# Kernel tuning notes

Hardware: AMD Instinct MI355X
Metric: run time of the kernel (lower is better)

The kernel has to match this reference:

```python
import jax, jax.numpy as jnp
import numpy as np

B, T, U, V, C, K = 64, 800, 64, 60, 512, 10

def setup_inputs() -> dict:
    key = jax.random.key(0)
    ks = jax.random.split(key, 8)
    x = jax.random.normal(ks[0], (B, T, 3), dtype=jnp.float32)
    char_ids = jax.random.randint(ks[1], (B, U), 0, V)
    onehots = jax.nn.one_hot(char_ids, V, dtype=jnp.float32)  # [B,U,V]
    text_lens = jax.random.randint(ks[2], (B, 1), 32, U + 1).astype(jnp.float32)
    w_old = jnp.zeros((B, V), jnp.float32)
    kappa_old = jnp.zeros((B, K), jnp.float32)
    prev_h = jnp.zeros((B, C), jnp.float32)
    prev_c = jnp.zeros((B, C), jnp.float32)
    s = 0.08
    W_ih = jax.random.normal(ks[3], (4 * C, 3 + V), jnp.float32) * s
    W_hh = jax.random.normal(ks[4], (4 * C, C), jnp.float32) * s
    b_ih = jnp.zeros((4 * C,), jnp.float32)
    b_hh = jnp.zeros((4 * C,), jnp.float32)
    win_W = jax.random.normal(ks[5], (3 * K, C), jnp.float32) * s
    win_b = jnp.zeros((3 * K,), jnp.float32)
    return dict(x=x, onehots=onehots, text_lens=text_lens, w_old=w_old,
                kappa_old=kappa_old, prev_h=prev_h, prev_c=prev_c,
                W_ih=W_ih, W_hh=W_hh, b_ih=b_ih, b_hh=b_hh,
                win_W=win_W, win_b=win_b)

def reference(x, onehots, text_lens, w_old, kappa_old, prev_h, prev_c,
              W_ih, W_hh, b_ih, b_hh, win_W, win_b):
    Upad = onehots.shape[1]
    idx = jnp.arange(Upad + 1, dtype=x.dtype)          # text-position indices
    scale = Upad / text_lens                           # [B,1] length normalization

    def step(carry, xt):
        h, c, w, kap = carry
        inp = jnp.concatenate([xt, w], axis=-1)        # [B, 3+V]
        gates = inp @ W_ih.T + b_ih + h @ W_hh.T + b_hh
        i, f, g, o = jnp.split(gates, 4, axis=-1)
        i = jax.nn.sigmoid(i); f = jax.nn.sigmoid(f)
        g = jnp.tanh(g);      o = jax.nn.sigmoid(o)
        c = f * c + i * g
        h = o * jnp.tanh(c)
        # Gaussian-mixture attention window
        p = jnp.exp(h @ win_W.T + win_b)               # [B, 3K]
        alpha, beta, dkap = jnp.split(p, 3, axis=-1)   # each [B, K]
        kap = kap + dkap
        gravity = -beta[:, :, None] * (kap[:, :, None] - idx) ** 2   # [B,K,U+1]
        phi = jnp.sum(alpha[:, :, None] * jnp.exp(gravity), axis=1) * scale  # [B,U+1]
        w = jnp.einsum('bu,buv->bv', phi[:, :Upad], onehots)
        return (h, c, w, kap), (h, w, phi)

    xs = jnp.swapaxes(x, 0, 1)                         # [T,B,3]
    (h, c, w, kap), (hs, ws, phis) = jax.lax.scan(
        step, (prev_h, prev_c, w_old, kappa_old), xs)
    ws = jnp.swapaxes(ws, 0, 1)                        # [B,T,V]
    hs = jnp.swapaxes(hs, 0, 1)                        # [B,T,C]
    return ws, hs, h, c, w, kap, phis[-1]
```

## Files before the change

kernel.cpp:

```cpp
#include <hip/hip_runtime.h>
#include <math.h>

#define B_  64
#define T_  800
#define U_  64
#define V_  60
#define C_  512
#define K_  10
#define KXF 584
#define NWG 256
#define NTH 512
#define KQ  8
#define KSL 72
#define NB  4
#define GRPWG 16

typedef unsigned long long ull;
typedef _Float16 f16;
typedef _Float16 f16x2 __attribute__((ext_vector_type(2)));

__device__ __forceinline__ float sigm(float v)  { return 1.f/(1.f+__expf(-v)); }
__device__ __forceinline__ float tanhx(float v) { return 1.f - 2.f/(__expf(2.f*v)+1.f); }

__device__ __forceinline__ ull ldp(const ull* p) {
  return __hip_atomic_load(p, __ATOMIC_RELAXED, __HIP_MEMORY_SCOPE_AGENT);
}
__device__ __forceinline__ float dot2(f16x2 a, f16x2 b, float c) {
  return __builtin_amdgcn_fdot2(a, b, c, false);
}
__device__ __forceinline__ f16x2 bc2(unsigned u) {
  return __builtin_bit_cast(f16x2, u);
}
__device__ __forceinline__ float wfetch(const float* __restrict__ W_ih,
                                        const float* __restrict__ W_hh,
                                        int row, int k) {
  if (k < 3)  return W_ih[row*63 + k];
  if (k == 3) return 0.f;
  if (k < 64) return W_ih[row*63 + (k-1)];
  return W_hh[row*C_ + (k-64)];
}

__global__ __launch_bounds__(NTH, 2)
void lstm_attn_persistent(
    const float* __restrict__ x,
    const float* __restrict__ onehots,
    const float* __restrict__ text_lens,
    const float* __restrict__ w_old,
    const float* __restrict__ kappa_old,
    const float* __restrict__ prev_h,
    const float* __restrict__ prev_c,
    const float* __restrict__ W_ih,
    const float* __restrict__ W_hh,
    const float* __restrict__ b_ih,
    const float* __restrict__ b_hh,
    const float* __restrict__ win_W,
    const float* __restrict__ win_b,
    ull* __restrict__ hpair,
    float* __restrict__ out)
{
  const long OUT_WS  = 0;
  const long OUT_HS  = (long)B_*T_*V_;
  const long OUT_H   = OUT_HS + (long)B_*T_*C_;
  const long OUT_C   = OUT_H  + (long)B_*C_;
  const long OUT_W   = OUT_C  + (long)B_*C_;
  const long OUT_KAP = OUT_W  + (long)B_*V_;
  const long OUT_PHI = OUT_KAP+ (long)B_*K_;

  const int tid  = threadIdx.x;
  const int kq   = tid >> 6;
  const int lane = tid & 63;
  const int bid  = blockIdx.x;
  const int grp  = bid & 15;
  const int gblk = bid >> 4;
  const int b0   = grp * NB;

  const int rlo = kq ? (kq*KSL - 64) : 0;
  const int rhi = kq*64 + 64;

  __shared__ __align__(16) f16   hxh[NB][KXF];
  __shared__ __align__(16) float wbuf[NB][64];
  __shared__ __align__(16) float part[KQ][NB][2][68];
  __shared__ __align__(16) float wpart[KQ][NB][68];
  __shared__ float p_lds[NB][32];
  __shared__ float kap_lds[NB][12];
  __shared__ float scale_lds[NB];
  __shared__ float winb_lds[32];
  __shared__ int   ids_lds[NB][64];

  f16x2 Wh[2][KSL/2];
  float bias2[2];
  #pragma unroll
  for (int s = 0; s < 2; ++s) {
    int gp   = gblk*128 + lane + 64*s;
    int gate = gp & 3;
    int ch   = gp >> 2;
    int row  = gate*C_ + ch;
    #pragma unroll
    for (int i = 0; i < KSL/2; ++i) {
      float w0 = wfetch(W_ih, W_hh, row, kq*KSL + 2*i);
      float w1 = wfetch(W_ih, W_hh, row, kq*KSL + 2*i + 1);
      f16x2 p; p[0] = (f16)w0; p[1] = (f16)w1;
      Wh[s][i] = p;
    }
    bias2[s] = b_ih[row] + b_hh[row];
  }

  const int wj = lane % 30;
  const int wh = (lane < 60) ? (lane / 30) : 0;
  f16x2 winh[16];
  #pragma unroll
  for (int i = 0; i < 16; ++i) {
    f16x2 p;
    p[0] = (f16)win_W[wj*C_ + kq*64 + wh*32 + 2*i];
    p[1] = (f16)win_W[wj*C_ + kq*64 + wh*32 + 2*i + 1];
    winh[i] = p;
  }

  const int ub    = tid >> 5;
  const int chloc = tid & 31;
  const int mych  = gblk*32 + chloc;
  float c_reg = 0.f;
  if (tid < 128) c_reg = prev_c[(long)(b0 + ub)*C_ + mych];

  for (int i = tid; i < NB*576; i += NTH) {
    int bb = i / 576, k = i % 576;
    int b = b0 + bb;
    float v;
    if      (k < 3)  v = x[((long)b*T_ + 0)*3 + k];
    else if (k < 4)  v = 0.f;
    else if (k < 64) v = w_old[b*V_ + (k-4)];
    else             v = prev_h[(long)b*C_ + (k-64)];
    hxh[bb][k] = (f16)v;
  }
  for (int i = tid; i < NB*64; i += NTH) {
    int bb = i >> 6, j = i & 63;
    wbuf[bb][j] = (j < 60) ? w_old[(b0+bb)*V_ + j] : 0.f;
  }
  for (int i = tid; i < NB*K_; i += NTH)
    kap_lds[i/K_][i%K_] = kappa_old[(b0 + i/K_)*K_ + i%K_];
  if (tid < NB) scale_lds[tid] = (float)U_ / text_lens[b0 + tid];
  if (tid < 30) winb_lds[tid] = win_b[tid];
  for (int i = tid; i < NB*U_; i += NTH) {
    int bb = i / U_, u = i % U_;
    const float* oh = onehots + ((long)(b0+bb)*U_ + u)*V_;
    int best = 0; float bv = oh[0];
    for (int vv = 1; vv < V_; ++vv) { float q = oh[vv]; if (q > bv) { bv = q; best = vv; } }
    ids_lds[bb][u] = best;
  }
  __syncthreads();

  for (int t = 0; t < T_; ++t) {
    float acc[NB][2];
    #pragma unroll
    for (int bb = 0; bb < NB; ++bb) {
      acc[bb][0] = (kq == 0) ? bias2[0] : 0.f;
      acc[bb][1] = (kq == 0) ? bias2[1] : 0.f;
    }
    #pragma unroll
    for (int bb = 0; bb < NB; ++bb) {
      const uint4* hb = (const uint4*)&hxh[bb][kq*KSL];
      float a0 = acc[bb][0], a1 = acc[bb][1];
      #pragma unroll
      for (int j = 0; j < 9; ++j) {
        uint4 hv = hb[j];
        f16x2 h0 = bc2(hv.x), h1 = bc2(hv.y), h2 = bc2(hv.z), h3 = bc2(hv.w);
        a0 = dot2(Wh[0][4*j+0], h0, a0);  a1 = dot2(Wh[1][4*j+0], h0, a1);
        a0 = dot2(Wh[0][4*j+1], h1, a0);  a1 = dot2(Wh[1][4*j+1], h1, a1);
        a0 = dot2(Wh[0][4*j+2], h2, a0);  a1 = dot2(Wh[1][4*j+2], h2, a1);
        a0 = dot2(Wh[0][4*j+3], h3, a0);  a1 = dot2(Wh[1][4*j+3], h3, a1);
      }
      acc[bb][0] = a0; acc[bb][1] = a1;
    }
    #pragma unroll
    for (int bb = 0; bb < NB; ++bb) {
      part[kq][bb][0][lane] = acc[bb][0];
      part[kq][bb][1][lane] = acc[bb][1];
    }
    __syncthreads();

    if (tid < 128) {
      const int sr = chloc >> 4, c4 = (chloc & 15) * 4;
      float4 s = make_float4(0.f, 0.f, 0.f, 0.f);
      #pragma unroll
      for (int q = 0; q < KQ; ++q) {
        float4 v = *(const float4*)&part[q][ub][sr][c4];
        s.x += v.x; s.y += v.y; s.z += v.z; s.w += v.w;
      }
      float ig = sigm(s.x), fg = sigm(s.y), gg = tanhx(s.z), og = sigm(s.w);
      float c = fg*c_reg + ig*gg;
      c_reg = c;
      float h = og * tanhx(c);
      int b = b0 + ub;
      ull pk = ((ull)(unsigned)(t+1) << 32) | (ull)__float_as_uint(h);
      __hip_atomic_store(&hpair[(long)(t&1)*B_*C_ + (long)b*C_ + mych], pk,
                         __ATOMIC_RELAXED, __HIP_MEMORY_SCOPE_AGENT);
      out[OUT_HS + ((long)b*T_ + t)*C_ + mych] = h;
      if (t == T_-1) {
        out[OUT_H + (long)b*C_ + mych] = h;
        out[OUT_C + (long)b*C_ + mych] = c;
      }
    }

    {
      const ull* src = hpair + (long)(t&1)*B_*C_;
      const int want = t + 1;
      const int ch = rlo + lane*2;
      const bool act = ch < rhi;
      const ull* q0 = src + (long)(b0+0)*C_ + ch;
      const ull* q1 = src + (long)(b0+1)*C_ + ch;
      const ull* q2 = src + (long)(b0+2)*C_ + ch;
      const ull* q3 = src + (long)(b0+3)*C_ + ch;
      ull a0=0,a1=0,c0=0,c1=0,e0=0,e1=0,g0=0,g1=0;
      while (true) {
        bool ok = true;
        if (act) {
          a0 = ldp(q0); a1 = ldp(q0+1);
          c0 = ldp(q1); c1 = ldp(q1+1);
          e0 = ldp(q2); e1 = ldp(q2+1);
          g0 = ldp(q3); g1 = ldp(q3+1);
          ok = (int)(a0>>32) >= want && (int)(a1>>32) >= want &&
               (int)(c0>>32) >= want && (int)(c1>>32) >= want &&
               (int)(e0>>32) >= want && (int)(e1>>32) >= want &&
               (int)(g0>>32) >= want && (int)(g1>>32) >= want;
        }
        if (__all(ok)) break;
      }
      if (act) {
        f16x2 p;
        p[0] = (f16)__uint_as_float((unsigned)a0);
        p[1] = (f16)__uint_as_float((unsigned)a1);
        *(unsigned*)&hxh[0][64+ch] = __builtin_bit_cast(unsigned, p);
        p[0] = (f16)__uint_as_float((unsigned)c0);
        p[1] = (f16)__uint_as_float((unsigned)c1);
        *(unsigned*)&hxh[1][64+ch] = __builtin_bit_cast(unsigned, p);
        p[0] = (f16)__uint_as_float((unsigned)e0);
        p[1] = (f16)__uint_as_float((unsigned)e1);
        *(unsigned*)&hxh[2][64+ch] = __builtin_bit_cast(unsigned, p);
        p[0] = (f16)__uint_as_float((unsigned)g0);
        p[1] = (f16)__uint_as_float((unsigned)g1);
        *(unsigned*)&hxh[3][64+ch] = __builtin_bit_cast(unsigned, p);
      }
    }

    #pragma unroll
    for (int bb = 0; bb < NB; ++bb) {
      const uint4* hb = (const uint4*)&hxh[bb][64 + kq*64 + wh*32];
      float a = 0.f;
      #pragma unroll
      for (int j = 0; j < 4; ++j) {
        uint4 hv = hb[j];
        a = dot2(winh[4*j+0], bc2(hv.x), a);
        a = dot2(winh[4*j+1], bc2(hv.y), a);
        a = dot2(winh[4*j+2], bc2(hv.z), a);
        a = dot2(winh[4*j+3], bc2(hv.w), a);
      }
      if (lane < 60) wpart[kq][bb][lane] = a;
    }
    __syncthreads();

    if (kq < NB) {
      const int bb = kq;
      if (lane < 30) {
        float s = 0.f;
        #pragma unroll
        for (int q = 0; q < KQ; ++q) s += wpart[q][bb][lane] + wpart[q][bb][30+lane];
        float p = __expf(s + winb_lds[lane]);
        p_lds[bb][lane] = p;
        if (lane >= 20) {
          float nk = kap_lds[bb][lane-20] + p;
          kap_lds[bb][lane-20] = nk;
          if (t == T_-1 && gblk == 0) out[OUT_KAP + (b0+bb)*K_ + (lane-20)] = nk;
        }
      }
      if (lane < 60) wbuf[bb][lane] = 0.f;
      else if (lane < 63) {
        int tn = t + 1;
        hxh[bb][lane-60] = (f16)((tn < T_) ? x[((long)(b0+bb)*T_ + tn)*3 + (lane-60)] : 0.f);
      }
      {
        float s = 0.f;
        float uf = (float)lane;
        #pragma unroll
        for (int k = 0; k < K_; ++k) {
          float d = kap_lds[bb][k] - uf;
          s += p_lds[bb][k] * __expf(-p_lds[bb][10+k]*d*d);
        }
        float phiv = s * scale_lds[bb];
        atomicAdd(&wbuf[bb][ids_lds[bb][lane]], phiv);
        if (t == T_-1 && gblk == 0) {
          out[OUT_PHI + (b0+bb)*65 + lane] = phiv;
          if (lane == 0) {
            float s2 = 0.f;
            #pragma unroll
            for (int k = 0; k < K_; ++k) {
              float d = kap_lds[bb][k] - 64.f;
              s2 += p_lds[bb][k] * __expf(-p_lds[bb][10+k]*d*d);
            }
            out[OUT_PHI + (b0+bb)*65 + 64] = s2 * scale_lds[bb];
          }
        }
      }
      if (lane < 60) {
        float wv = wbuf[bb][lane];
        hxh[bb][4+lane] = (f16)wv;
        if (gblk == (t & 15)) {
          out[OUT_WS + ((long)(b0+bb)*T_ + t)*V_ + lane] = wv;
          if (t == T_-1) out[OUT_W + (b0+bb)*V_ + lane] = wv;
        }
      }
    }
    __syncthreads();
  }
}

extern "C" void kernel_launch(void* const* d_in, const int* in_sizes, int n_in,
                              void* d_out, int out_size, void* d_ws, size_t ws_size,
                              hipStream_t stream) {
  const float* x         = (const float*)d_in[0];
  const float* onehots   = (const float*)d_in[1];
  const float* text_lens = (const float*)d_in[2];
  const float* w_old     = (const float*)d_in[3];
  const float* kappa_old = (const float*)d_in[4];
  const float* prev_h    = (const float*)d_in[5];
  const float* prev_c    = (const float*)d_in[6];
  const float* W_ih      = (const float*)d_in[7];
  const float* W_hh      = (const float*)d_in[8];
  const float* b_ih      = (const float*)d_in[9];
  const float* b_hh      = (const float*)d_in[10];
  const float* win_W     = (const float*)d_in[11];
  const float* win_b     = (const float*)d_in[12];
  ull*   hpair = (ull*)d_ws;
  float* out   = (float*)d_out;

  hipMemsetAsync(d_ws, 0, 2ull*B_*C_*sizeof(ull), stream);

  lstm_attn_persistent<<<NWG, NTH, 0, stream>>>(
      x, onehots, text_lens, w_old, kappa_old, prev_h, prev_c,
      W_ih, W_hh, b_ih, b_hh, win_W, win_b, hpair, out);
}
```

Before: 4.326 ms.

## Poll hidden-state exchange via XCD-local L2 with MALL fallback copy

Each h value is now written twice, once as a plain store to a local copy and once as an agent-scope atomic to a global copy. Consumers poll with inline-asm dwordx4 loads that carry sc0 (local L2 scope) and switch permanently to sc0 sc1 loads of the global copy after 200 failed tries. The goal is cheaper polling when producer and consumer share an XCD, plus vectorized 16-byte loads that replace eight separate 8-byte atomic loads. In exchange it doubles the h stores and the workspace, and correctness depends on the fallback path, since plain stores from another XCD may not become visible in the local L2.

```diff
diff --git a/kernel.cpp b/kernel.cpp
--- a/kernel.cpp
+++ b/kernel.cpp
@@ -19,12 +19,11 @@
 typedef _Float16 f16;
 typedef _Float16 f16x2 __attribute__((ext_vector_type(2)));
 
+#define HL_N (2*B_*C_)
+
 __device__ __forceinline__ float sigm(float v)  { return 1.f/(1.f+__expf(-v)); }
 __device__ __forceinline__ float tanhx(float v) { return 1.f - 2.f/(__expf(2.f*v)+1.f); }
 
-__device__ __forceinline__ ull ldp(const ull* p) {
-  return __hip_atomic_load(p, __ATOMIC_RELAXED, __HIP_MEMORY_SCOPE_AGENT);
-}
 __device__ __forceinline__ float dot2(f16x2 a, f16x2 b, float c) {
   return __builtin_amdgcn_fdot2(a, b, c, false);
 }
@@ -38,6 +37,33 @@
   if (k == 3) return 0.f;
   if (k < 64) return W_ih[row*63 + (k-1)];
   return W_hh[row*C_ + (k-64)];
+}
+
+__device__ __forceinline__ void ld4x16_loc(const ull* p0, const ull* p1,
+                                           const ull* p2, const ull* p3,
+                                           ulonglong2& r0, ulonglong2& r1,
+                                           ulonglong2& r2, ulonglong2& r3) {
+  asm volatile(
+    "global_load_dwordx4 %0, %4, off sc0\n\t"
+    "global_load_dwordx4 %1, %5, off sc0\n\t"
+    "global_load_dwordx4 %2, %6, off sc0\n\t"
+    "global_load_dwordx4 %3, %7, off sc0\n\t"
+    "s_waitcnt vmcnt(0)"
+    : "=&v"(r0), "=&v"(r1), "=&v"(r2), "=&v"(r3)
+    : "v"(p0), "v"(p1), "v"(p2), "v"(p3) : "memory");
+}
+__device__ __forceinline__ void ld4x16_mal(const ull* p0, const ull* p1,
+                                           const ull* p2, const ull* p3,
+                                           ulonglong2& r0, ulonglong2& r1,
+                                           ulonglong2& r2, ulonglong2& r3) {
+  asm volatile(
+    "global_load_dwordx4 %0, %4, off sc0 sc1\n\t"
+    "global_load_dwordx4 %1, %5, off sc0 sc1\n\t"
+    "global_load_dwordx4 %2, %6, off sc0 sc1\n\t"
+    "global_load_dwordx4 %3, %7, off sc0 sc1\n\t"
+    "s_waitcnt vmcnt(0)"
+    : "=&v"(r0), "=&v"(r1), "=&v"(r2), "=&v"(r3)
+    : "v"(p0), "v"(p1), "v"(p2), "v"(p3) : "memory");
 }
 
 __global__ __launch_bounds__(NTH, 2)
@@ -55,9 +81,11 @@
     const float* __restrict__ b_hh,
     const float* __restrict__ win_W,
     const float* __restrict__ win_b,
-    ull* __restrict__ hpair,
+    ull* __restrict__ hl,
     float* __restrict__ out)
 {
+  __builtin_amdgcn_fence(__ATOMIC_ACQUIRE, "agent");
+
   const long OUT_WS  = 0;
   const long OUT_HS  = (long)B_*T_*V_;
   const long OUT_H   = OUT_HS + (long)B_*T_*C_;
@@ -65,6 +93,8 @@
   const long OUT_W   = OUT_C  + (long)B_*C_;
   const long OUT_KAP = OUT_W  + (long)B_*V_;
   const long OUT_PHI = OUT_KAP+ (long)B_*K_;
+
+  ull* hg = hl + HL_N;
 
   const int tid  = threadIdx.x;
   const int kq   = tid >> 6;
@@ -148,6 +178,8 @@
     ids_lds[bb][u] = best;
   }
   __syncthreads();
+
+  bool use_mall = false;
 
   for (int t = 0; t < T_; ++t) {
     float acc[NB][2];
@@ -192,7 +224,9 @@
       float h = og * tanhx(c);
       int b = b0 + ub;
       ull pk = ((ull)(unsigned)(t+1) << 32) | (ull)__float_as_uint(h);
-      __hip_atomic_store(&hpair[(long)(t&1)*B_*C_ + (long)b*C_ + mych], pk,
+      long hidx = (long)(t&1)*B_*C_ + (long)b*C_ + mych;
+      hl[hidx] = pk;
+      __hip_atomic_store(&hg[hidx], pk,
                          __ATOMIC_RELAXED, __HIP_MEMORY_SCOPE_AGENT);
       out[OUT_HS + ((long)b*T_ + t)*C_ + mych] = h;
       if (t == T_-1) {
@@ -202,42 +236,44 @@
     }
 
     {
-      const ull* src = hpair + (long)(t&1)*B_*C_;
       const int want = t + 1;
       const int ch = rlo + lane*2;
       const bool act = ch < rhi;
-      const ull* q0 = src + (long)(b0+0)*C_ + ch;
-      const ull* q1 = src + (long)(b0+1)*C_ + ch;
-      const ull* q2 = src + (long)(b0+2)*C_ + ch;
-      const ull* q3 = src + (long)(b0+3)*C_ + ch;
-      ull a0=0,a1=0,c0=0,c1=0,e0=0,e1=0,g0=0,g1=0;
+      const long boff = (long)(t&1)*B_*C_ + ch;
+      ulonglong2 r0, r1, r2, r3;
+      r0.x=r0.y=r1.x=r1.y=r2.x=r2.y=r3.x=r3.y=0;
+      int tries = 0;
       while (true) {
         bool ok = true;
         if (act) {
-          a0 = ldp(q0); a1 = ldp(q0+1);
-          c0 = ldp(q1); c1 = ldp(q1+1);
-          e0 = ldp(q2); e1 = ldp(q2+1);
-          g0 = ldp(q3); g1 = ldp(q3+1);
-          ok = (int)(a0>>32) >= want && (int)(a1>>32) >= want &&
-               (int)(c0>>32) >= want && (int)(c1>>32) >= want &&
-               (int)(e0>>32) >= want && (int)(e1>>32) >= want &&
-               (int)(g0>>32) >= want && (int)(g1>>32) >= want;
+          const ull* base = use_mall ? hg : hl;
+          const ull* p0 = base + boff + (long)(b0+0)*C_;
+          const ull* p1 = base + boff + (long)(b0+1)*C_;
+          const ull* p2 = base + boff + (long)(b0+2)*C_;
+          const ull* p3 = base + boff + (long)(b0+3)*C_;
+          if (use_mall) ld4x16_mal(p0,p1,p2,p3, r0,r1,r2,r3);
+          else          ld4x16_loc(p0,p1,p2,p3, r0,r1,r2,r3);
+          ok = (int)(r0.x>>32) >= want && (int)(r0.y>>32) >= want &&
+               (int)(r1.x>>32) >= want && (int)(r1.y>>32) >= want &&
+               (int)(r2.x>>32) >= want && (int)(r2.y>>32) >= want &&
+               (int)(r3.x>>32) >= want && (int)(r3.y>>32) >= want;
         }
         if (__all(ok)) break;
+        if (!use_mall && ++tries > 200) use_mall = true;
       }
       if (act) {
         f16x2 p;
-        p[0] = (f16)__uint_as_float((unsigned)a0);
-        p[1] = (f16)__uint_as_float((unsigned)a1);
+        p[0] = (f16)__uint_as_float((unsigned)r0.x);
+        p[1] = (f16)__uint_as_float((unsigned)r0.y);
         *(unsigned*)&hxh[0][64+ch] = __builtin_bit_cast(unsigned, p);
-        p[0] = (f16)__uint_as_float((unsigned)c0);
-        p[1] = (f16)__uint_as_float((unsigned)c1);
+        p[0] = (f16)__uint_as_float((unsigned)r1.x);
+        p[1] = (f16)__uint_as_float((unsigned)r1.y);
         *(unsigned*)&hxh[1][64+ch] = __builtin_bit_cast(unsigned, p);
-        p[0] = (f16)__uint_as_float((unsigned)e0);
-        p[1] = (f16)__uint_as_float((unsigned)e1);
+        p[0] = (f16)__uint_as_float((unsigned)r2.x);
+        p[1] = (f16)__uint_as_float((unsigned)r2.y);
         *(unsigned*)&hxh[2][64+ch] = __builtin_bit_cast(unsigned, p);
-        p[0] = (f16)__uint_as_float((unsigned)g0);
-        p[1] = (f16)__uint_as_float((unsigned)g1);
+        p[0] = (f16)__uint_as_float((unsigned)r3.x);
+        p[1] = (f16)__uint_as_float((unsigned)r3.y);
         *(unsigned*)&hxh[3][64+ch] = __builtin_bit_cast(unsigned, p);
       }
     }
@@ -329,12 +365,12 @@
   const float* b_hh      = (const float*)d_in[10];
   const float* win_W     = (const float*)d_in[11];
   const float* win_b     = (const float*)d_in[12];
-  ull*   hpair = (ull*)d_ws;
-  float* out   = (float*)d_out;
-
-  hipMemsetAsync(d_ws, 0, 2ull*B_*C_*sizeof(ull), stream);
+  ull*   hl  = (ull*)d_ws;
+  float* out = (float*)d_out;
+
+  hipMemsetAsync(d_ws, 0, 2ull*HL_N*sizeof(ull), stream);
 
   lstm_attn_persistent<<<NWG, NTH, 0, stream>>>(
       x, onehots, text_lens, w_old, kappa_old, prev_h, prev_c,
-      W_ih, W_hh, b_ih, b_hh, win_W, win_b, hpair, out);
-}
+      W_ih, W_hh, b_ih, b_hh, win_W, win_b, hl, out);
+}
```

Result: faster. 4.116 ms (-4.9%).

## Split batch across twice as many workgroups and poll h with coherent vector loads

Applied to the files above, without the earlier changes.

Halves the batch rows per workgroup (NB 4→2) and doubles the grid to 512 persistent workgroups in 32 groups, raising launch bounds to 4 blocks per CU. Each workgroup then does half the per-step recurrent dot-product work, shortening the serial per-step critical path. It also replaces eight scalar relaxed atomic loads in the spin-wait with two 16-byte global loads carrying cache-bypass bits (sc0 sc1) via inline asm. This doubles the number of cross-workgroup pollers, adds more global polling traffic, and needs all 512 workgroups co-resident for the spin-wait to be safe.

```diff
diff --git a/kernel.cpp b/kernel.cpp
--- a/kernel.cpp
+++ b/kernel.cpp
@@ -8,11 +8,12 @@
 #define C_  512
 #define K_  10
 #define KXF 584
-#define NWG 256
+#define NWG 512
 #define NTH 512
 #define KQ  8
 #define KSL 72
-#define NB  4
+#define NB  2
+#define NGRP 32
 #define GRPWG 16
 
 typedef unsigned long long ull;
@@ -22,9 +23,6 @@
 __device__ __forceinline__ float sigm(float v)  { return 1.f/(1.f+__expf(-v)); }
 __device__ __forceinline__ float tanhx(float v) { return 1.f - 2.f/(__expf(2.f*v)+1.f); }
 
-__device__ __forceinline__ ull ldp(const ull* p) {
-  return __hip_atomic_load(p, __ATOMIC_RELAXED, __HIP_MEMORY_SCOPE_AGENT);
-}
 __device__ __forceinline__ float dot2(f16x2 a, f16x2 b, float c) {
   return __builtin_amdgcn_fdot2(a, b, c, false);
 }
@@ -40,7 +38,17 @@
   return W_hh[row*C_ + (k-64)];
 }
 
-__global__ __launch_bounds__(NTH, 2)
+__device__ __forceinline__ void ld2x16_mal(const ull* p0, const ull* p1,
+                                           ulonglong2& r0, ulonglong2& r1) {
+  asm volatile(
+    "global_load_dwordx4 %0, %2, off sc0 sc1\n\t"
+    "global_load_dwordx4 %1, %3, off sc0 sc1\n\t"
+    "s_waitcnt vmcnt(0)"
+    : "=&v"(r0), "=&v"(r1)
+    : "v"(p0), "v"(p1) : "memory");
+}
+
+__global__ __launch_bounds__(NTH, 4)
 void lstm_attn_persistent(
     const float* __restrict__ x,
     const float* __restrict__ onehots,
@@ -70,8 +78,8 @@
   const int kq   = tid >> 6;
   const int lane = tid & 63;
   const int bid  = blockIdx.x;
-  const int grp  = bid & 15;
-  const int gblk = bid >> 4;
+  const int grp  = bid & 31;
+  const int gblk = bid >> 5;
   const int b0   = grp * NB;
 
   const int rlo = kq ? (kq*KSL - 64) : 0;
@@ -120,7 +128,7 @@
   const int chloc = tid & 31;
   const int mych  = gblk*32 + chloc;
   float c_reg = 0.f;
-  if (tid < 128) c_reg = prev_c[(long)(b0 + ub)*C_ + mych];
+  if (tid < 64) c_reg = prev_c[(long)(b0 + ub)*C_ + mych];
 
   for (int i = tid; i < NB*576; i += NTH) {
     int bb = i / 576, k = i % 576;
@@ -178,7 +186,7 @@
     }
     __syncthreads();
 
-    if (tid < 128) {
+    if (tid < 64) {
       const int sr = chloc >> 4, c4 = (chloc & 15) * 4;
       float4 s = make_float4(0.f, 0.f, 0.f, 0.f);
       #pragma unroll
@@ -202,43 +210,31 @@
     }
 
     {
-      const ull* src = hpair + (long)(t&1)*B_*C_;
       const int want = t + 1;
       const int ch = rlo + lane*2;
       const bool act = ch < rhi;
-      const ull* q0 = src + (long)(b0+0)*C_ + ch;
-      const ull* q1 = src + (long)(b0+1)*C_ + ch;
-      const ull* q2 = src + (long)(b0+2)*C_ + ch;
-      const ull* q3 = src + (long)(b0+3)*C_ + ch;
-      ull a0=0,a1=0,c0=0,c1=0,e0=0,e1=0,g0=0,g1=0;
+      const long boff = (long)(t&1)*B_*C_ + ch;
+      ulonglong2 r0, r1;
+      r0.x=r0.y=r1.x=r1.y=0;
       while (true) {
         bool ok = true;
         if (act) {
-          a0 = ldp(q0); a1 = ldp(q0+1);
-          c0 = ldp(q1); c1 = ldp(q1+1);
-          e0 = ldp(q2); e1 = ldp(q2+1);
-          g0 = ldp(q3); g1 = ldp(q3+1);
-          ok = (int)(a0>>32) >= want && (int)(a1>>32) >= want &&
-               (int)(c0>>32) >= want && (int)(c1>>32) >= want &&
-               (int)(e0>>32) >= want && (int)(e1>>32) >= want &&
-               (int)(g0>>32) >= want && (int)(g1>>32) >= want;
+          const ull* p0 = hpair + boff + (long)(b0+0)*C_;
+          const ull* p1 = hpair + boff + (long)(b0+1)*C_;
+          ld2x16_mal(p0, p1, r0, r1);
+          ok = (int)(r0.x>>32) >= want && (int)(r0.y>>32) >= want &&
+               (int)(r1.x>>32) >= want && (int)(r1.y>>32) >= want;
         }
         if (__all(ok)) break;
       }
       if (act) {
         f16x2 p;
-        p[0] = (f16)__uint_as_float((unsigned)a0);
-        p[1] = (f16)__uint_as_float((unsigned)a1);
+        p[0] = (f16)__uint_as_float((unsigned)r0.x);
+        p[1] = (f16)__uint_as_float((unsigned)r0.y);
         *(unsigned*)&hxh[0][64+ch] = __builtin_bit_cast(unsigned, p);
-        p[0] = (f16)__uint_as_float((unsigned)c0);
-        p[1] = (f16)__uint_as_float((unsigned)c1);
+        p[0] = (f16)__uint_as_float((unsigned)r1.x);
+        p[1] = (f16)__uint_as_float((unsigned)r1.y);
         *(unsigned*)&hxh[1][64+ch] = __builtin_bit_cast(unsigned, p);
-        p[0] = (f16)__uint_as_float((unsigned)e0);
-        p[1] = (f16)__uint_as_float((unsigned)e1);
-        *(unsigned*)&hxh[2][64+ch] = __builtin_bit_cast(unsigned, p);
-        p[0] = (f16)__uint_as_float((unsigned)g0);
-        p[1] = (f16)__uint_as_float((unsigned)g1);
-        *(unsigned*)&hxh[3][64+ch] = __builtin_bit_cast(unsigned, p);
       }
     }
 
```

New measurement: 5.249 ms. 21.3% more time.
